# Optimization experiments

Measured on AMD Instinct MI355X. Metric: run time of the kernel, lower is better.

The kernel has to match this reference:

```python
import jax, jax.numpy as jnp
import numpy as np
from jax import lax

H = 64
IN = 3

def _lstm_layer(x, Wih, Whh, bih, bhh, collect):
    # x: [B, T, in]; Wih: [4H, in]; Whh: [4H, H]. PyTorch gate order: i, f, g, o.
    B = x.shape[0]
    h0 = jnp.zeros((B, H), x.dtype)
    c0 = jnp.zeros((B, H), x.dtype)
    b = bih + bhh
    def step(carry, xt):
        h, c = carry
        gates = xt @ Wih.T + h @ Whh.T + b  # [B, 4H]
        i, f, g, o = jnp.split(gates, 4, axis=-1)
        i = jax.nn.sigmoid(i); f = jax.nn.sigmoid(f)
        g = jnp.tanh(g); o = jax.nn.sigmoid(o)
        c = f * c + i * g
        h = o * jnp.tanh(c)
        return (h, c), (h if collect else None)
    xs = jnp.swapaxes(x, 0, 1)  # [T, B, in]
    (h, c), hs = lax.scan(step, (h0, c0), xs)
    if collect:
        return jnp.swapaxes(hs, 0, 1)  # [B, T, H]
    return h  # [B, H]


def setup_inputs() -> dict:
    key = jax.random.key(0)
    ks = jax.random.split(key, 14)
    s = 1.0 / np.sqrt(H)
    def u(k, shape):
        return jax.random.uniform(k, shape, jnp.float32, -s, s)
    return {
        "x": jax.random.normal(ks[0], (4096, 512, IN), jnp.float32),
        "Wih0": u(ks[1], (4 * H, IN)), "Whh0": u(ks[2], (4 * H, H)),
        "bih0": u(ks[3], (4 * H,)), "bhh0": u(ks[4], (4 * H,)),
        "Wih1": u(ks[5], (4 * H, H)), "Whh1": u(ks[6], (4 * H, H)),
        "bih1": u(ks[7], (4 * H,)), "bhh1": u(ks[8], (4 * H,)),
        "Wc1": jax.random.normal(ks[9], (32, H), jnp.float32) * 0.1,
        "bc1": jnp.zeros((32,), jnp.float32),
        "Wc2": jax.random.normal(ks[10], (1, 32), jnp.float32) * 0.1,
        "bc2": jnp.zeros((1,), jnp.float32),
    }


def reference(x, Wih0, Whh0, bih0, bhh0, Wih1, Whh1, bih1, bhh1, Wc1, bc1, Wc2, bc2):
    # 2-layer LSTM (dropout inactive at inference); only last timestep of layer 2 is used.
    h1 = _lstm_layer(x, Wih0, Whh0, bih0, bhh0, collect=True)   # [B, T, H]
    last = _lstm_layer(h1, Wih1, Whh1, bih1, bhh1, collect=False)  # [B, H]
    hidden = jax.nn.relu(last @ Wc1.T + bc1)  # [B, 32]
    out = jax.nn.sigmoid(hidden @ Wc2.T + bc2)  # [B, 1]
    return out
```

## Files before the change

kernel.cpp:

```cpp
#include <hip/hip_runtime.h>

#define TSEQ   512
#define BATCH  4096
#define MROWS  16

typedef short bf16x8 __attribute__((ext_vector_type(8)));
typedef float f32x4  __attribute__((ext_vector_type(4)));
typedef float f32x2  __attribute__((ext_vector_type(2)));

#define NL2E  (-1.44269504f)
#define P2L2E (2.88539008f)

__device__ __forceinline__ unsigned short f2bf(float f) {
    unsigned int u = __builtin_bit_cast(unsigned int, f);
    return (unsigned short)((u + 0x8000u) >> 16);
}

__device__ __forceinline__ f32x2 cellupd2(const f32x4 a, const f32x4 b, f32x2& C) {
    f32x2 ei = {__builtin_amdgcn_exp2f(a[0]), __builtin_amdgcn_exp2f(b[0])};
    f32x2 ef = {__builtin_amdgcn_exp2f(a[1]), __builtin_amdgcn_exp2f(b[1])};
    f32x2 eg = {__builtin_amdgcn_exp2f(a[2]), __builtin_amdgcn_exp2f(b[2])};
    f32x2 eo = {__builtin_amdgcn_exp2f(a[3]), __builtin_amdgcn_exp2f(b[3])};
    f32x2 A  = 1.f + ei;
    f32x2 G1 = eg + 1.f;
    f32x2 F  = 1.f + ef;
    f32x2 t  = A * G1;
    f32x2 G2 = eg * P2L2E + (NL2E * 2.f);
    f32x2 num = C * t + G2 * F;
    f32x2 den = t * F;
    f32x2 r  = {__builtin_amdgcn_rcpf(den.x), __builtin_amdgcn_rcpf(den.y)};
    f32x2 Cn = num * r;
    Cn.x = fminf(Cn.x, 126.f);
    Cn.y = fminf(Cn.y, 126.f);
    C = Cn;
    f32x2 ec = {__builtin_amdgcn_exp2f(Cn.x), __builtin_amdgcn_exp2f(Cn.y)};
    f32x2 B  = 1.f + eo;
    f32x2 hn = ec - 1.f;
    f32x2 hd = B * (ec + 1.f);
    f32x2 rr = {__builtin_amdgcn_rcpf(hd.x), __builtin_amdgcn_rcpf(hd.y)};
    return hn * rr;
}


__global__ __launch_bounds__(512, 2) void lstm2_kernel(
    const float* __restrict__ x,
    const float* __restrict__ Wih0, const float* __restrict__ Whh0,
    const float* __restrict__ bih0, const float* __restrict__ bhh0,
    const float* __restrict__ Wih1, const float* __restrict__ Whh1,
    const float* __restrict__ bih1, const float* __restrict__ bhh1,
    const float* __restrict__ Wc1,  const float* __restrict__ bc1,
    const float* __restrict__ Wc2,  const float* __restrict__ bc2,
    float* __restrict__ out)
{
    __shared__ __align__(16) unsigned short ring[2][MROWS * 64];
    __shared__ __align__(16) unsigned short h2s[2][MROWS * 64];
    __shared__ __align__(16) unsigned short xq[64][128];
    __shared__ float h2f[MROWS][65];
    __shared__ float hid[MROWS][33];

    const int tid  = threadIdx.x;
    const int wv   = tid >> 6;
    const int lane = tid & 63;
    const int col  = lane & 15;
    const int lg   = lane >> 4;
    const int b0   = blockIdx.x * MROWS;
    const int sw   = (col & 7) << 4;

    for (int i = tid; i < 1024; i += 512) {
        ((unsigned int*)ring)[i] = 0u;
        ((unsigned int*)h2s)[i]  = 0u;
    }

    const int xrow = tid >> 5;
    const int xt   = tid & 31;
    const float* xb = x + ((size_t)(b0 + xrow) * TSEQ + xt) * 3;
    float xr0 = xb[0], xr1 = xb[1], xr2 = xb[2];
    {
        bf16x8 xf = {(short)f2bf(xr0),(short)f2bf(xr1),(short)f2bf(xr2),0,0,0,0,0};
        *(bf16x8*)((char*)xq + (xt << 8) + ((xrow << 4) ^ ((xt & 7) << 4))) = xf;
    }
    xr0 = xb[96]; xr1 = xb[97]; xr2 = xb[98];
    __syncthreads();

    const int rd0 = (col * 128 +      lg * 16) ^ sw;
    const int rd1 = (col * 128 + 64 + lg * 16) ^ sw;

#define FLUSH(S) do { \
    if (((S) & 31) == 16 && (S) < 480) { \
        const int c1_ = ((S) >> 5) + 1; \
        const int t64_ = ((c1_ & 1) << 5) + xt; \
        bf16x8 xf_ = {(short)f2bf(xr0),(short)f2bf(xr1),(short)f2bf(xr2),0,0,0,0,0}; \
        *(bf16x8*)((char*)xq + (t64_ << 8) + ((xrow << 4) ^ ((xt & 7) << 4))) = xf_; \
        if (c1_ < 15) { const float* p_ = xb + (c1_ + 1) * 96; xr0 = p_[0]; xr1 = p_[1]; xr2 = p_[2]; } \
    } \
} while(0)

#define XQRD(S) (*(const bf16x8*)((const char*)xq + ((((S)&63)) << 8) + ((col << 4) ^ (((S)&7) << 4))))
#define MM(A,B,C) __builtin_amdgcn_mfma_f32_16x16x32_bf16((A),(B),(C),0,0,0)

    const int wq = wv;
    const int ga = col & 3;
    const float sca = (ga == 2) ? P2L2E : NL2E;
    bf16x8 WfL1[2][3];
    f32x4 biaL1[2];
#pragma unroll
    for (int tt = 0; tt < 2; ++tt) {
        const int n = ga * 64 + 16 * (col >> 2) + 2 * wq + tt;
#pragma unroll
        for (int f = 0; f < 3; ++f)
#pragma unroll
            for (int i = 0; i < 8; ++i) {
                const int k = f * 32 + lg * 8 + i;
                float v = 0.f;
                if (k < 64)      v = Whh0[n * 64 + k];
                else if (k < 67) v = Wih0[n * 3 + (k - 64)];
                WfL1[tt][f][i] = (short)f2bf(sca * v);
            }
#pragma unroll
        for (int r = 0; r < 4; ++r) {
            const int nb = r * 64 + 16 * lg + 2 * wq + tt;
            biaL1[tt][r] = ((r == 2) ? P2L2E : NL2E) * (bih0[nb] + bhh0[nb]);
        }
    }
    bf16x8 WfL2[2][4];
    f32x4 biaL2[2];
#pragma unroll
    for (int tt = 0; tt < 2; ++tt) {
        const int n = ga * 64 + 16 * (col >> 2) + 2 * wq + tt;
#pragma unroll
        for (int f = 0; f < 4; ++f)
#pragma unroll
            for (int i = 0; i < 8; ++i) {
                const int k = f * 32 + lg * 8 + i;
                const float v = (k < 64) ? Wih1[n * 64 + k] : Whh1[n * 64 + (k - 64)];
                WfL2[tt][f][i] = (short)f2bf(sca * v);
            }
#pragma unroll
        for (int r = 0; r < 4; ++r) {
            const int nb = r * 64 + 16 * lg + 2 * wq + tt;
            biaL2[tt][r] = ((r == 2) ? P2L2E : NL2E) * (bih1[nb] + bhh1[nb]);
        }
    }
    const int hw = (col * 128 + 32 * lg + 4 * wq) ^ sw;
    f32x2 C_L1 = {0.f, 0.f};
    f32x2 C_L2 = {0.f, 0.f};
    f32x2 hv01 = {0.f, 0.f};
    bf16x8 pv2 = XQRD(0);

#define MRG(P, S) do { \
        const char* rb_ = (const char*)ring[P]; \
        const char* hp_ = (const char*)h2s[(P) ^ 1]; \
        bf16x8 v0_ = *(const bf16x8*)(rb_ + rd0); \
        bf16x8 v1_ = *(const bf16x8*)(rb_ + rd1); \
        bf16x8 v2_ = *(const bf16x8*)(hp_ + rd0); \
        bf16x8 v3_ = *(const bf16x8*)(hp_ + rd1); \
        f32x4 b0_ = MM(WfL1[0][2], pv2, biaL1[0]); \
        f32x4 b1_ = MM(WfL1[1][2], pv2, biaL1[1]); \
        b0_ = MM(WfL1[0][0], v0_, b0_); \
        b1_ = MM(WfL1[1][0], v0_, b1_); \
        f32x4 c0_ = MM(WfL2[0][0], v0_, biaL2[0]); \
        f32x4 c1_ = MM(WfL2[1][0], v0_, biaL2[1]); \
        b0_ = MM(WfL1[0][1], v1_, b0_); \
        b1_ = MM(WfL1[1][1], v1_, b1_); \
        pv2 = XQRD((S) + 1); \
        f32x2 hL1_ = cellupd2(b0_, b1_, C_L1); \
        c0_ = MM(WfL2[0][1], v1_, c0_); \
        c1_ = MM(WfL2[1][1], v1_, c1_); \
        c0_ = MM(WfL2[0][2], v2_, c0_); \
        c1_ = MM(WfL2[1][2], v2_, c1_); \
        c0_ = MM(WfL2[0][3], v3_, c0_); \
        c1_ = MM(WfL2[1][3], v3_, c1_); \
        unsigned int p0_; \
        asm("v_cvt_pk_bf16_f32 %0, %1, %2" : "=v"(p0_) : "v"(hL1_.x), "v"(hL1_.y)); \
        *(unsigned int*)((char*)ring[(P) ^ 1] + hw) = p0_; \
        hv01 = cellupd2(c0_, c1_, C_L2); \
        unsigned int p1_; \
        asm("v_cvt_pk_bf16_f32 %0, %1, %2" : "=v"(p1_) : "v"(hv01.x), "v"(hv01.y)); \
        *(unsigned int*)((char*)h2s[P] + hw) = p1_; \
    } while(0)

    {
        const char* rb_ = (const char*)ring[1];
        bf16x8 v0_ = *(const bf16x8*)(rb_ + rd0);
        bf16x8 v1_ = *(const bf16x8*)(rb_ + rd1);
        f32x4 b0_ = MM(WfL1[0][2], pv2, biaL1[0]);
        f32x4 b1_ = MM(WfL1[1][2], pv2, biaL1[1]);
        b0_ = MM(WfL1[0][0], v0_, b0_);
        b1_ = MM(WfL1[1][0], v0_, b1_);
        b0_ = MM(WfL1[0][1], v1_, b0_);
        b1_ = MM(WfL1[1][1], v1_, b1_);
        pv2 = XQRD(1);
        f32x2 hL1_ = cellupd2(b0_, b1_, C_L1);
        unsigned int p0_;
        asm("v_cvt_pk_bf16_f32 %0, %1, %2" : "=v"(p0_) : "v"(hL1_.x), "v"(hL1_.y));
        *(unsigned int*)((char*)ring[0] + hw) = p0_;
    }
    __syncthreads();

#pragma unroll 1
    for (int m = 0; m < 255; ++m) {
        MRG(0, 2 * m + 1);
        __syncthreads();
        FLUSH(2 * m + 2);
        MRG(1, 2 * m + 2);
        __syncthreads();
    }
    MRG(0, 511);
    __syncthreads();

    {
        const char* rb_ = (const char*)ring[1];
        const char* hp_ = (const char*)h2s[0];
        bf16x8 v0_ = *(const bf16x8*)(rb_ + rd0);
        bf16x8 v1_ = *(const bf16x8*)(rb_ + rd1);
        bf16x8 v2_ = *(const bf16x8*)(hp_ + rd0);
        bf16x8 v3_ = *(const bf16x8*)(hp_ + rd1);
        f32x4 c0_ = MM(WfL2[0][0], v0_, biaL2[0]);
        f32x4 c1_ = MM(WfL2[1][0], v0_, biaL2[1]);
        c0_ = MM(WfL2[0][1], v1_, c0_);
        c1_ = MM(WfL2[1][1], v1_, c1_);
        c0_ = MM(WfL2[0][2], v2_, c0_);
        c1_ = MM(WfL2[1][2], v2_, c1_);
        c0_ = MM(WfL2[0][3], v3_, c0_);
        c1_ = MM(WfL2[1][3], v3_, c1_);
        hv01 = cellupd2(c0_, c1_, C_L2);
    }
    const int ub = 16 * lg + 2 * wq;
    h2f[col][ub + 0] = hv01.x;
    h2f[col][ub + 1] = hv01.y;
    __syncthreads();

    {
        const int b = tid & 15, j = tid >> 4;
        float s = bc1[j];
#pragma unroll 8
        for (int k = 0; k < 64; ++k) s += Wc1[j * 64 + k] * h2f[b][k];
        hid[b][j] = fmaxf(s, 0.f);
    }
    __syncthreads();
    if (tid < 16) {
        float s = bc2[0];
#pragma unroll 8
        for (int k = 0; k < 32; ++k) s += Wc2[k] * hid[tid][k];
        float e = __builtin_amdgcn_exp2f(NL2E * s);
        out[b0 + tid] = __builtin_amdgcn_rcpf(1.f + e);
    }
}

extern "C" void kernel_launch(void* const* d_in, const int* in_sizes, int n_in,
                              void* d_out, int out_size, void* d_ws, size_t ws_size,
                              hipStream_t stream) {
    lstm2_kernel<<<BATCH / MROWS, 512, 0, stream>>>(
        (const float*)d_in[0],
        (const float*)d_in[1], (const float*)d_in[2],
        (const float*)d_in[3], (const float*)d_in[4],
        (const float*)d_in[5], (const float*)d_in[6],
        (const float*)d_in[7], (const float*)d_in[8],
        (const float*)d_in[9], (const float*)d_in[10],
        (const float*)d_in[11], (const float*)d_in[12],
        (float*)d_out);
}
```

Measured before the change: 326.4 us.

## Split LSTM layers into producer/consumer wavegroups with LDS counter barriers

Doubles the block to 1024 threads, with 8 waves running layer 1 and 8 waves running layer 2. The two halves synchronise through LDS atomic counters and a 4-slot ring of layer-1 hidden states instead of block-wide __syncthreads. The aim is to let the two recurrences run concurrently as a pipeline and to replace full barriers with lighter counter waits. In exchange it adds spin-wait overhead with s_sleep, more waves per CU with higher register pressure, and ordering risks in the hand-written barrier protocol.

```diff
diff --git a/kernel.cpp b/kernel.cpp
--- a/kernel.cpp
+++ b/kernel.cpp
@@ -42,7 +42,18 @@
 }
 
 
-__global__ __launch_bounds__(512, 2) void lstm2_kernel(
+__device__ __forceinline__ void waitcnt_ge(int* c, int tgt) {
+    if (__hip_atomic_load(c, __ATOMIC_ACQUIRE, __HIP_MEMORY_SCOPE_WORKGROUP) >= tgt) return;
+    do { __builtin_amdgcn_s_sleep(1); }
+    while (__hip_atomic_load(c, __ATOMIC_ACQUIRE, __HIP_MEMORY_SCOPE_WORKGROUP) < tgt);
+}
+__device__ __forceinline__ void bar_signal(int* c, int lane) {
+    asm volatile("s_waitcnt lgkmcnt(0)" ::: "memory");
+    if (lane == 0)
+        __hip_atomic_fetch_add(c, 1, __ATOMIC_RELEASE, __HIP_MEMORY_SCOPE_WORKGROUP);
+}
+
+__global__ __launch_bounds__(1024, 4) void lstm2_kernel(
     const float* __restrict__ x,
     const float* __restrict__ Wih0, const float* __restrict__ Whh0,
     const float* __restrict__ bih0, const float* __restrict__ bhh0,
@@ -52,11 +63,12 @@
     const float* __restrict__ Wc2,  const float* __restrict__ bc2,
     float* __restrict__ out)
 {
-    __shared__ __align__(16) unsigned short ring[2][MROWS * 64];
+    __shared__ __align__(16) unsigned short ring[4][MROWS * 64];
     __shared__ __align__(16) unsigned short h2s[2][MROWS * 64];
     __shared__ __align__(16) unsigned short xq[64][128];
     __shared__ float h2f[MROWS][65];
     __shared__ float hid[MROWS][33];
+    __shared__ int cntL1, cntL2;
 
     const int tid  = threadIdx.x;
     const int wv   = tid >> 6;
@@ -66,20 +78,21 @@
     const int b0   = blockIdx.x * MROWS;
     const int sw   = (col & 7) << 4;
 
-    for (int i = tid; i < 1024; i += 512) {
-        ((unsigned int*)ring)[i] = 0u;
-        ((unsigned int*)h2s)[i]  = 0u;
-    }
-
-    const int xrow = tid >> 5;
+    ((unsigned int*)ring)[tid]        = 0u;
+    ((unsigned int*)ring)[tid + 1024] = 0u;
+    ((unsigned int*)h2s)[tid]         = 0u;
+    if (tid == 0) { cntL1 = 0; cntL2 = 0; }
+
+    const int xrow = (tid >> 5) & 15;
     const int xt   = tid & 31;
     const float* xb = x + ((size_t)(b0 + xrow) * TSEQ + xt) * 3;
-    float xr0 = xb[0], xr1 = xb[1], xr2 = xb[2];
-    {
+    float xr0 = 0.f, xr1 = 0.f, xr2 = 0.f;
+    if (tid < 512) {
+        xr0 = xb[0]; xr1 = xb[1]; xr2 = xb[2];
         bf16x8 xf = {(short)f2bf(xr0),(short)f2bf(xr1),(short)f2bf(xr2),0,0,0,0,0};
         *(bf16x8*)((char*)xq + (xt << 8) + ((xrow << 4) ^ ((xt & 7) << 4))) = xf;
-    }
-    xr0 = xb[96]; xr1 = xb[97]; xr2 = xb[98];
+        xr0 = xb[96]; xr1 = xb[97]; xr2 = xb[98];
+    }
     __syncthreads();
 
     const int rd0 = (col * 128 +      lg * 16) ^ sw;
@@ -98,139 +111,135 @@
 #define XQRD(S) (*(const bf16x8*)((const char*)xq + ((((S)&63)) << 8) + ((col << 4) ^ (((S)&7) << 4))))
 #define MM(A,B,C) __builtin_amdgcn_mfma_f32_16x16x32_bf16((A),(B),(C),0,0,0)
 
-    const int wq = wv;
-    const int ga = col & 3;
-    const float sca = (ga == 2) ? P2L2E : NL2E;
-    bf16x8 WfL1[2][3];
-    f32x4 biaL1[2];
-#pragma unroll
-    for (int tt = 0; tt < 2; ++tt) {
-        const int n = ga * 64 + 16 * (col >> 2) + 2 * wq + tt;
-#pragma unroll
-        for (int f = 0; f < 3; ++f)
-#pragma unroll
-            for (int i = 0; i < 8; ++i) {
-                const int k = f * 32 + lg * 8 + i;
-                float v = 0.f;
-                if (k < 64)      v = Whh0[n * 64 + k];
-                else if (k < 67) v = Wih0[n * 3 + (k - 64)];
-                WfL1[tt][f][i] = (short)f2bf(sca * v);
+    if (wv < 8) {
+        const int wq = wv;
+        const int ga = col & 3;
+        const float sca = (ga == 2) ? P2L2E : NL2E;
+        bf16x8 WfL1[2][3];
+        f32x4 biaL1[2];
+#pragma unroll
+        for (int tt = 0; tt < 2; ++tt) {
+            const int n = ga * 64 + 16 * (col >> 2) + 2 * wq + tt;
+#pragma unroll
+            for (int f = 0; f < 3; ++f)
+#pragma unroll
+                for (int i = 0; i < 8; ++i) {
+                    const int k = f * 32 + lg * 8 + i;
+                    float v = 0.f;
+                    if (k < 64)      v = Whh0[n * 64 + k];
+                    else if (k < 67) v = Wih0[n * 3 + (k - 64)];
+                    WfL1[tt][f][i] = (short)f2bf(sca * v);
+                }
+#pragma unroll
+            for (int r = 0; r < 4; ++r) {
+                const int nb = r * 64 + 16 * lg + 2 * wq + tt;
+                biaL1[tt][r] = ((r == 2) ? P2L2E : NL2E) * (bih0[nb] + bhh0[nb]);
             }
-#pragma unroll
-        for (int r = 0; r < 4; ++r) {
-            const int nb = r * 64 + 16 * lg + 2 * wq + tt;
-            biaL1[tt][r] = ((r == 2) ? P2L2E : NL2E) * (bih0[nb] + bhh0[nb]);
-        }
-    }
-    bf16x8 WfL2[2][4];
-    f32x4 biaL2[2];
-#pragma unroll
-    for (int tt = 0; tt < 2; ++tt) {
-        const int n = ga * 64 + 16 * (col >> 2) + 2 * wq + tt;
-#pragma unroll
-        for (int f = 0; f < 4; ++f)
-#pragma unroll
-            for (int i = 0; i < 8; ++i) {
-                const int k = f * 32 + lg * 8 + i;
-                const float v = (k < 64) ? Wih1[n * 64 + k] : Whh1[n * 64 + (k - 64)];
-                WfL2[tt][f][i] = (short)f2bf(sca * v);
-            }
-#pragma unroll
-        for (int r = 0; r < 4; ++r) {
-            const int nb = r * 64 + 16 * lg + 2 * wq + tt;
-            biaL2[tt][r] = ((r == 2) ? P2L2E : NL2E) * (bih1[nb] + bhh1[nb]);
-        }
-    }
-    const int hw = (col * 128 + 32 * lg + 4 * wq) ^ sw;
-    f32x2 C_L1 = {0.f, 0.f};
-    f32x2 C_L2 = {0.f, 0.f};
-    f32x2 hv01 = {0.f, 0.f};
-    bf16x8 pv2 = XQRD(0);
-
-#define MRG(P, S) do { \
-        const char* rb_ = (const char*)ring[P]; \
-        const char* hp_ = (const char*)h2s[(P) ^ 1]; \
+        }
+        const int hw = (col * 128 + 32 * lg + 4 * wq) ^ sw;
+        f32x2 C01 = {0.f, 0.f};
+        bf16x8 pv2 = XQRD(0);
+        int tg = 8;
+
+#define L1STEP(PS, WS, SS, BP) do { \
+        const char* rb_ = (const char*)ring[PS]; \
         bf16x8 v0_ = *(const bf16x8*)(rb_ + rd0); \
         bf16x8 v1_ = *(const bf16x8*)(rb_ + rd1); \
-        bf16x8 v2_ = *(const bf16x8*)(hp_ + rd0); \
-        bf16x8 v3_ = *(const bf16x8*)(hp_ + rd1); \
         f32x4 b0_ = MM(WfL1[0][2], pv2, biaL1[0]); \
         f32x4 b1_ = MM(WfL1[1][2], pv2, biaL1[1]); \
         b0_ = MM(WfL1[0][0], v0_, b0_); \
         b1_ = MM(WfL1[1][0], v0_, b1_); \
+        b0_ = MM(WfL1[0][1], v1_, b0_); \
+        b1_ = MM(WfL1[1][1], v1_, b1_); \
+        pv2 = XQRD((SS) + 1); \
+        f32x2 h01_ = cellupd2(b0_, b1_, C01); \
+        unsigned int p0_; \
+        asm("v_cvt_pk_bf16_f32 %0, %1, %2" : "=v"(p0_) : "v"(h01_.x), "v"(h01_.y)); \
+        if (BP) waitcnt_ge(&cntL2, tg - 32); \
+        *(unsigned int*)((char*)ring[WS] + hw) = p0_; \
+        bar_signal(&cntL1, lane); \
+        waitcnt_ge(&cntL1, tg); \
+        tg += 8; \
+    } while(0)
+
+#pragma unroll 1
+        for (int q = 0; q < 128; ++q) {
+            const int tq = 4 * q;
+            FLUSH(tq);
+            L1STEP(3, 0, tq,     q);
+            L1STEP(0, 1, tq + 1, q);
+            L1STEP(2 - 1, 2, tq + 2, q);
+            L1STEP(2, 3, tq + 3, q);
+        }
+#undef L1STEP
+    } else {
+        const int wq = wv - 8;
+        const int ga = col & 3;
+        const float sca = (ga == 2) ? P2L2E : NL2E;
+        bf16x8 WfL2[2][4];
+        f32x4 biaL2[2];
+#pragma unroll
+        for (int tt = 0; tt < 2; ++tt) {
+            const int n = ga * 64 + 16 * (col >> 2) + 2 * wq + tt;
+#pragma unroll
+            for (int f = 0; f < 4; ++f)
+#pragma unroll
+                for (int i = 0; i < 8; ++i) {
+                    const int k = f * 32 + lg * 8 + i;
+                    const float v = (k < 64) ? Wih1[n * 64 + k] : Whh1[n * 64 + (k - 64)];
+                    WfL2[tt][f][i] = (short)f2bf(sca * v);
+                }
+#pragma unroll
+            for (int r = 0; r < 4; ++r) {
+                const int nb = r * 64 + 16 * lg + 2 * wq + tt;
+                biaL2[tt][r] = ((r == 2) ? P2L2E : NL2E) * (bih1[nb] + bhh1[nb]);
+            }
+        }
+        const int hw2 = (col * 128 + 32 * lg + 4 * wq) ^ sw;
+        f32x2 C01 = {0.f, 0.f};
+        f32x2 hv01 = {0.f, 0.f};
+        int tg = 8;
+
+#define L2STEP(RS, HR, HWS) do { \
+        const char* hp_ = (const char*)h2s[HR]; \
+        bf16x8 v2_ = *(const bf16x8*)(hp_ + rd0); \
+        bf16x8 v3_ = *(const bf16x8*)(hp_ + rd1); \
+        waitcnt_ge(&cntL1, tg); \
+        const char* rb_ = (const char*)ring[RS]; \
+        bf16x8 v0_ = *(const bf16x8*)(rb_ + rd0); \
+        bf16x8 v1_ = *(const bf16x8*)(rb_ + rd1); \
         f32x4 c0_ = MM(WfL2[0][0], v0_, biaL2[0]); \
         f32x4 c1_ = MM(WfL2[1][0], v0_, biaL2[1]); \
-        b0_ = MM(WfL1[0][1], v1_, b0_); \
-        b1_ = MM(WfL1[1][1], v1_, b1_); \
-        pv2 = XQRD((S) + 1); \
-        f32x2 hL1_ = cellupd2(b0_, b1_, C_L1); \
         c0_ = MM(WfL2[0][1], v1_, c0_); \
         c1_ = MM(WfL2[1][1], v1_, c1_); \
         c0_ = MM(WfL2[0][2], v2_, c0_); \
         c1_ = MM(WfL2[1][2], v2_, c1_); \
         c0_ = MM(WfL2[0][3], v3_, c0_); \
         c1_ = MM(WfL2[1][3], v3_, c1_); \
-        unsigned int p0_; \
-        asm("v_cvt_pk_bf16_f32 %0, %1, %2" : "=v"(p0_) : "v"(hL1_.x), "v"(hL1_.y)); \
-        *(unsigned int*)((char*)ring[(P) ^ 1] + hw) = p0_; \
-        hv01 = cellupd2(c0_, c1_, C_L2); \
+        hv01 = cellupd2(c0_, c1_, C01); \
         unsigned int p1_; \
         asm("v_cvt_pk_bf16_f32 %0, %1, %2" : "=v"(p1_) : "v"(hv01.x), "v"(hv01.y)); \
-        *(unsigned int*)((char*)h2s[P] + hw) = p1_; \
+        *(unsigned int*)((char*)h2s[HWS] + hw2) = p1_; \
+        bar_signal(&cntL2, lane); \
+        waitcnt_ge(&cntL2, tg); \
+        tg += 8; \
     } while(0)
 
-    {
-        const char* rb_ = (const char*)ring[1];
-        bf16x8 v0_ = *(const bf16x8*)(rb_ + rd0);
-        bf16x8 v1_ = *(const bf16x8*)(rb_ + rd1);
-        f32x4 b0_ = MM(WfL1[0][2], pv2, biaL1[0]);
-        f32x4 b1_ = MM(WfL1[1][2], pv2, biaL1[1]);
-        b0_ = MM(WfL1[0][0], v0_, b0_);
-        b1_ = MM(WfL1[1][0], v0_, b1_);
-        b0_ = MM(WfL1[0][1], v1_, b0_);
-        b1_ = MM(WfL1[1][1], v1_, b1_);
-        pv2 = XQRD(1);
-        f32x2 hL1_ = cellupd2(b0_, b1_, C_L1);
-        unsigned int p0_;
-        asm("v_cvt_pk_bf16_f32 %0, %1, %2" : "=v"(p0_) : "v"(hL1_.x), "v"(hL1_.y));
-        *(unsigned int*)((char*)ring[0] + hw) = p0_;
+#pragma unroll 1
+        for (int q = 0; q < 128; ++q) {
+            L2STEP(0, 1, 0);
+            L2STEP(1, 0, 1);
+            L2STEP(2, 1, 0);
+            L2STEP(3, 0, 1);
+        }
+#undef L2STEP
+        const int ub = 16 * lg + 2 * wq;
+        h2f[col][ub + 0] = hv01.x;
+        h2f[col][ub + 1] = hv01.y;
     }
     __syncthreads();
 
-#pragma unroll 1
-    for (int m = 0; m < 255; ++m) {
-        MRG(0, 2 * m + 1);
-        __syncthreads();
-        FLUSH(2 * m + 2);
-        MRG(1, 2 * m + 2);
-        __syncthreads();
-    }
-    MRG(0, 511);
-    __syncthreads();
-
-    {
-        const char* rb_ = (const char*)ring[1];
-        const char* hp_ = (const char*)h2s[0];
-        bf16x8 v0_ = *(const bf16x8*)(rb_ + rd0);
-        bf16x8 v1_ = *(const bf16x8*)(rb_ + rd1);
-        bf16x8 v2_ = *(const bf16x8*)(hp_ + rd0);
-        bf16x8 v3_ = *(const bf16x8*)(hp_ + rd1);
-        f32x4 c0_ = MM(WfL2[0][0], v0_, biaL2[0]);
-        f32x4 c1_ = MM(WfL2[1][0], v0_, biaL2[1]);
-        c0_ = MM(WfL2[0][1], v1_, c0_);
-        c1_ = MM(WfL2[1][1], v1_, c1_);
-        c0_ = MM(WfL2[0][2], v2_, c0_);
-        c1_ = MM(WfL2[1][2], v2_, c1_);
-        c0_ = MM(WfL2[0][3], v3_, c0_);
-        c1_ = MM(WfL2[1][3], v3_, c1_);
-        hv01 = cellupd2(c0_, c1_, C_L2);
-    }
-    const int ub = 16 * lg + 2 * wq;
-    h2f[col][ub + 0] = hv01.x;
-    h2f[col][ub + 1] = hv01.y;
-    __syncthreads();
-
-    {
+    if (tid < 512) {
         const int b = tid & 15, j = tid >> 4;
         float s = bc1[j];
 #pragma unroll 8
@@ -250,7 +259,7 @@
 extern "C" void kernel_launch(void* const* d_in, const int* in_sizes, int n_in,
                               void* d_out, int out_size, void* d_ws, size_t ws_size,
                               hipStream_t stream) {
-    lstm2_kernel<<<BATCH / MROWS, 512, 0, stream>>>(
+    lstm2_kernel<<<BATCH / MROWS, 1024, 0, stream>>>(
         (const float*)d_in[0],
         (const float*)d_in[1], (const float*)d_in[2],
         (const float*)d_in[3], (const float*)d_in[4],
```

Measured after the change: 391.9 us. 20.1% more time.
